# Kernel optimization log

Hardware: AMD Instinct MI355X
Metric: run time of the kernel (lower is better)

Reference implementation:

```python
import jax, jax.numpy as jnp
import numpy as np

H = 16        # num_heads
D = 64        # head_dim
HID = 1024    # hidden_size
WIN = 256     # window_size
GLOBAL = 0    # single global token index {0}


def _rope_tables(L):
    inv_freq = 1.0 / (10000.0 ** (jnp.arange(0, D, 2, dtype=jnp.float32) / D))
    pos = jnp.arange(L, dtype=jnp.float32)
    freqs = pos[:, None] * inv_freq[None, :]          # [L, D/2]
    emb = jnp.concatenate([freqs, freqs], axis=-1)     # [L, D]
    return jnp.cos(emb), jnp.sin(emb)


def _apply_rope(x, cos, sin):
    # x: [B, H, L, D]; cos/sin: [L, D]
    x1, x2 = x[..., : D // 2], x[..., D // 2 :]
    rot = jnp.concatenate([-x2, x1], axis=-1)
    return x * cos[None, None] + rot * sin[None, None]


def setup_inputs() -> dict:
    key = jax.random.key(0)
    ks = jax.random.split(key, 6)
    B, L = 2, 2048
    s = 0.02
    return {
        "hidden_states": jax.random.normal(ks[0], (B, L, HID), jnp.float32),
        "q_w": jax.random.normal(ks[1], (HID, HID), jnp.float32) * s,
        "q_b": jnp.zeros((HID,), jnp.float32),
        "k_w": jax.random.normal(ks[2], (HID, HID), jnp.float32) * s,
        "k_b": jnp.zeros((HID,), jnp.float32),
        "v_w": jax.random.normal(ks[3], (HID, HID), jnp.float32) * s,
        "v_b": jnp.zeros((HID,), jnp.float32),
        "o_w": jax.random.normal(ks[4], (HID, HID), jnp.float32) * s,
        "o_b": jnp.zeros((HID,), jnp.float32),
    }


def reference(hidden_states, q_w, q_b, k_w, k_b, v_w, v_b, o_w, o_b):
    B, L, _ = hidden_states.shape
    # torch Linear: y = x @ W^T + b
    q = hidden_states @ q_w.T + q_b
    k = hidden_states @ k_w.T + k_b
    v = hidden_states @ v_w.T + v_b
    # [B, L, H*D] -> [B, H, L, D]
    q = q.reshape(B, L, H, D).transpose(0, 2, 1, 3)
    k = k.reshape(B, L, H, D).transpose(0, 2, 1, 3)
    v = v.reshape(B, L, H, D).transpose(0, 2, 1, 3)

    cos, sin = _rope_tables(L)
    q = _apply_rope(q, cos, sin)
    k = _apply_rope(k, cos, sin)

    scale = jnp.float32(np.sqrt(D))
    scores = jnp.einsum("bhid,bhjd->bhij", q, k) / scale  # [B, H, L, L]

    # sparse mask: causal AND (within sliding window OR global token)
    i = jnp.arange(L)[:, None]
    j = jnp.arange(L)[None, :]
    keep = (j <= i) & (((i - j) < WIN) | (j == GLOBAL))    # [L, L] bool
    scores = jnp.where(keep[None, None], scores, jnp.float32(-jnp.inf))

    probs = jax.nn.softmax(scores, axis=-1)
    out = jnp.einsum("bhij,bhjd->bhid", probs, v)           # [B, H, L, D]
    out = out.transpose(0, 2, 1, 3).reshape(B, L, HID)
    return out @ o_w.T + o_b
```

## Files before the change

kernel.cpp:

```cpp
#include <hip/hip_runtime.h>
#include <hip/hip_bf16.h>
#include <cstdint>

#define LSEQ   2048
#define HID    1024
#define WIN    256
#define MROWS  4096

typedef unsigned short u16;
typedef unsigned int   u32;
typedef __attribute__((ext_vector_type(8))) short bf16x8;
typedef __attribute__((ext_vector_type(4))) float f32x4;
typedef __attribute__((address_space(1))) const unsigned int as1_uint;
typedef __attribute__((address_space(3))) unsigned int as3_uint;
typedef __attribute__((address_space(3))) char as3_char;

static __device__ __forceinline__ float bf2f(u16 u) {
  union { u32 u; float f; } c; c.u = ((u32)u) << 16; return c.f;
}
static __device__ __forceinline__ u16 f2bf(float f) {
  union { float f; u32 u; } c; c.f = f;
  u32 r = c.u + 0x7fffu + ((c.u >> 16) & 1u);
  return (u16)(r >> 16);
}

__global__ void cvt_all(const float* __restrict__ hidden,
                        const float* __restrict__ qw, const float* __restrict__ kw,
                        const float* __restrict__ vw, const float* __restrict__ ow,
                        u16* __restrict__ hbf, u16* __restrict__ wbf,
                        float* __restrict__ tab) {
  const int b = blockIdx.x;
  if (b >= 8192) {
    const int idx = (b - 8192) * 256 + threadIdx.x;
    const int l = idx >> 5, d = idx & 31;
    float invf = exp2f(-(float)d * (13.287712379549449f / 32.0f));
    float ang = (float)l * invf;
    tab[l * 64 + 2 * d]     = cosf(ang);
    tab[l * 64 + 2 * d + 1] = sinf(ang);
    return;
  }
  const int i = b * 256 + threadIdx.x;
  const float* src; u16* dst; int off;
  if (i < (1 << 20)) {
    src = hidden; dst = hbf; off = i;
  } else {
    const int j = i - (1 << 20);
    const int seg = j >> 18;
    off = j & ((1 << 18) - 1);
    src = (seg == 0) ? qw : (seg == 1) ? kw : (seg == 2) ? vw : ow;
    dst = wbf + ((size_t)seg << 20);
  }
  float4 v = ((const float4*)src)[off];
  u32 lo = (u32)f2bf(v.x) | ((u32)f2bf(v.y) << 16);
  u32 hi = (u32)f2bf(v.z) | ((u32)f2bf(v.w) << 16);
  ((uint2*)dst)[off] = make_uint2(lo, hi);
}

template<int NW>
__global__ __launch_bounds__(256, 2) void gemm_bt(
    const u16* __restrict__ A, const u16* __restrict__ W,
    const float* __restrict__ b0, const float* __restrict__ b1, const float* __restrict__ b2,
    u16* __restrict__ outb, float* __restrict__ outf, const float* __restrict__ tab,
    u16* __restrict__ vt)
{
  __shared__ u16 As[128 * 64];
  __shared__ u16 Bs[128 * 64];
  const int tid = threadIdx.x;
  const int lane = tid & 63, w = tid >> 6;
  const int wr = w >> 1, wc = w & 1;
  const int c = lane & 15, g = lane >> 4;

  const int GX = (NW == 3) ? 24 : 8;
  const int CH = (GX * 32) >> 3;
  int fid = blockIdx.y * GX + blockIdx.x;
  fid = (fid & 7) * CH + (fid >> 3);
  const int bx = fid % GX, by = fid / GX;

  const int srow = tid >> 3;
  const int scolb = ((tid & 7) * 16) ^ ((srow & 7) << 4);
  const char* gA = (const char*)(A + (size_t)(by * 128 + srow) * HID) + scolb;
  const char* gB = (const char*)(W + (size_t)(bx * 128 + srow) * HID) + scolb;

  f32x4 acc[4][4] = {};

  for (int kt = 0; kt < HID; kt += 64) {
    __syncthreads();
    #pragma unroll
    for (int r = 0; r < 4; ++r) {
      __builtin_amdgcn_global_load_lds((as1_uint*)(gA + kt * 2 + r * 32 * (HID * 2)),
                                       (as3_uint*)((as3_char*)As + r * 4096 + w * 1024), 16, 0, 0);
      __builtin_amdgcn_global_load_lds((as1_uint*)(gB + kt * 2 + r * 32 * (HID * 2)),
                                       (as3_uint*)((as3_char*)Bs + r * 4096 + w * 1024), 16, 0, 0);
    }
    __syncthreads();

    const int sw = (c & 7) << 4;
    #pragma unroll
    for (int ks = 0; ks < 2; ++ks) {
      const int colb = (g * 16 + ks * 64);
      bf16x8 af[4], bfr[4];
      #pragma unroll
      for (int mm = 0; mm < 4; ++mm) {
        const int row = wr * 64 + mm * 16 + c;
        af[mm] = *(const bf16x8*)((const char*)As + row * 128 + (colb ^ sw));
      }
      #pragma unroll
      for (int nn = 0; nn < 4; ++nn) {
        const int row = wc * 64 + nn * 16 + c;
        bfr[nn] = *(const bf16x8*)((const char*)Bs + row * 128 + (colb ^ sw));
      }
      #pragma unroll
      for (int mm = 0; mm < 4; ++mm)
        #pragma unroll
        for (int nn = 0; nn < 4; ++nn)
          acc[mm][nn] = __builtin_amdgcn_mfma_f32_16x16x32_bf16(af[mm], bfr[nn], acc[mm][nn], 0, 0, 0);
    }
  }

  const int which = (NW == 3) ? (bx >> 3) : 0;
  const float* bp = (NW == 3) ? (which == 0 ? b0 : (which == 1 ? b1 : b2)) : b0;
  const int cb = (NW == 3) ? ((bx & 7) * 128) : bx * 128;
  u16* ob_ = (NW == 3) ? (outb + (size_t)which * MROWS * HID) : (u16*)nullptr;
  const int rowg = by * 128 + wr * 64;

  #pragma unroll
  for (int nn = 0; nn < 4; ++nn) {
    const float bias = bp[cb + wc * 64 + nn * 16 + c];
    #pragma unroll
    for (int mm = 0; mm < 4; ++mm)
      #pragma unroll
      for (int r = 0; r < 4; ++r) acc[mm][nn][r] += bias;
  }

  if (NW == 3 && which < 2) {
    const float QS = (which == 0) ? (0.125f * 1.4426950408889634f) : 1.0f;
    #pragma unroll
    for (int mm = 0; mm < 4; ++mm) {
      #pragma unroll
      for (int r = 0; r < 4; ++r) {
        const int l = (rowg + mm * 16 + (g << 2) + r) & (LSEQ - 1);
        const float2* trow = (const float2*)(tab + l * 64);
        const float2 t0 = trow[c];
        const float2 t1 = trow[c + 16];
        const float x0 = acc[mm][0][r], y0 = acc[mm][2][r];
        const float x1 = acc[mm][1][r], y1 = acc[mm][3][r];
        acc[mm][0][r] = (x0 * t0.x - y0 * t0.y) * QS;
        acc[mm][2][r] = (y0 * t0.x + x0 * t0.y) * QS;
        acc[mm][1][r] = (x1 * t1.x - y1 * t1.y) * QS;
        acc[mm][3][r] = (y1 * t1.x + x1 * t1.y) * QS;
      }
    }
  }

  if (NW == 3 && which == 2) {
    #pragma unroll
    for (int nn = 0; nn < 4; ++nn) {
      const int cl = cb + wc * 64 + nn * 16 + c;
      const int hh = cl >> 6, hd = cl & 63;
      #pragma unroll
      for (int mm = 0; mm < 4; ++mm) {
        const int rb = rowg + mm * 16 + (g << 2);
        const int b_ = rb >> 11, l = rb & (LSEQ - 1);
        u16 t4[4];
        #pragma unroll
        for (int r = 0; r < 4; ++r) t4[r] = f2bf(acc[mm][nn][r]);
        *(uint2*)&vt[(size_t)((b_ * 16 + hh) * 64 + hd) * LSEQ + l] = *(uint2*)t4;
      }
    }
  } else {
    #pragma unroll
    for (int nn = 0; nn < 4; ++nn) {
      const int cl = cb + wc * 64 + nn * 16 + c;
      #pragma unroll
      for (int mm = 0; mm < 4; ++mm) {
        const int rb = rowg + mm * 16 + (g << 2);
        #pragma unroll
        for (int r = 0; r < 4; ++r) {
          if (NW == 3) ob_[(size_t)(rb + r) * HID + cl] = f2bf(acc[mm][nn][r]);
          else         outf[(size_t)(rb + r) * HID + cl] = acc[mm][nn][r];
        }
      }
    }
  }
}

__global__ __launch_bounds__(256) void attn_mfma(
    const u16* __restrict__ Q, const u16* __restrict__ K,
    const u16* __restrict__ Vt, u16* __restrict__ O)
{
  __shared__ u16 Ks[2 * 64 * 64];
  __shared__ u16 Vs[2 * 64 * 64];
  __shared__ u16 Ps[4 * 16 * 64];

  const int tid = threadIdx.x, lane = tid & 63, w = tid >> 6;
  const int g = lane >> 4, c = lane & 15;
  const int qb = (blockIdx.x & 31) * 64;
  const int bh = blockIdx.x >> 5;
  const int h = bh & 15;
  const size_t row0 = (size_t)(bh >> 4) * LSEQ;
  const int qw = qb + w * 16;

  const int srow = (w << 4) + (lane >> 3);
  const int scol = ((lane & 7) * 16) ^ ((lane >> 3) << 4);
  const char* gKb = (const char*)(K + (row0 + srow) * HID + h * 64) + scol;
  const char* gVb = (const char*)(Vt + (size_t)(bh * 64 + srow) * LSEQ) + scol;

  const u16* qptr = Q + (row0 + qw + c) * HID + h * 64 + g * 8;
  bf16x8 qa0 = *(const bf16x8*)qptr;
  bf16x8 qa1 = *(const bf16x8*)(qptr + 32);

  const int cbk = qb >> 6;
  int cf = (qb - (WIN - 1)) >> 6; if (cf < 0) cf = 0;

  float psum[4] = {0.f, 0.f, 0.f, 0.f};
  f32x4 o_[4];
  #pragma unroll
  for (int dt = 0; dt < 4; ++dt) o_[dt] = f32x4{0.f, 0.f, 0.f, 0.f};

  if (cf > 0) {
    const u16* k0p = K + row0 * HID + h * 64 + g * 8;
    bf16x8 k0a = *(const bf16x8*)k0p;
    bf16x8 k0b = *(const bf16x8*)(k0p + 32);
    float part = 0.f;
    #pragma unroll
    for (int j = 0; j < 8; ++j)
      part += bf2f((u16)qa0[j]) * bf2f((u16)k0a[j]) + bf2f((u16)qa1[j]) * bf2f((u16)k0b[j]);
    part += __shfl_xor(part, 16);
    part += __shfl_xor(part, 32);
    float p0 = exp2f(part);
    float prs[4];
    #pragma unroll
    for (int r = 0; r < 4; ++r) { prs[r] = __shfl(p0, g * 4 + r); psum[r] = prs[r]; }
    #pragma unroll
    for (int dt = 0; dt < 4; ++dt) {
      float v0 = bf2f(Vt[(size_t)(bh * 64 + dt * 16 + c) * LSEQ]);
      #pragma unroll
      for (int r = 0; r < 4; ++r) o_[dt][r] = prs[r] * v0;
    }
  }

  {
    const size_t kadv = (size_t)cf * 64 * 2048;
    const size_t vadv = (size_t)cf * 128;
    as3_char* lk = (as3_char*)Ks + w * 2048;
    as3_char* lv = (as3_char*)Vs + w * 2048;
    __builtin_amdgcn_global_load_lds((as1_uint*)(gKb + kadv),         (as3_uint*)lk,          16, 0, 0);
    __builtin_amdgcn_global_load_lds((as1_uint*)(gKb + kadv + 16384), (as3_uint*)(lk + 1024), 16, 0, 0);
    __builtin_amdgcn_global_load_lds((as1_uint*)(gVb + vadv),         (as3_uint*)lv,          16, 0, 0);
    __builtin_amdgcn_global_load_lds((as1_uint*)(gVb + vadv + 32768), (as3_uint*)(lv + 1024), 16, 0, 0);
  }

  int buf = 0;
  for (int ci = cf; ci <= cbk; ++ci) {
    const int c0 = ci * 64;
    __syncthreads();

    if (ci < cbk) {
      const size_t kadv = (size_t)(c0 + 64) * 2048;
      const size_t vadv = (size_t)(c0 + 64) * 2;
      as3_char* lk = (as3_char*)Ks + (buf ^ 1) * 8192 + w * 2048;
      as3_char* lv = (as3_char*)Vs + (buf ^ 1) * 8192 + w * 2048;
      __builtin_amdgcn_global_load_lds((as1_uint*)(gKb + kadv),         (as3_uint*)lk,          16, 0, 0);
      __builtin_amdgcn_global_load_lds((as1_uint*)(gKb + kadv + 16384), (as3_uint*)(lk + 1024), 16, 0, 0);
      __builtin_amdgcn_global_load_lds((as1_uint*)(gVb + vadv),         (as3_uint*)lv,          16, 0, 0);
      __builtin_amdgcn_global_load_lds((as1_uint*)(gVb + vadv + 32768), (as3_uint*)(lv + 1024), 16, 0, 0);
    }

    const char* ksbase = (const char*)Ks + buf * 8192;
    const char* vsbase = (const char*)Vs + buf * 8192;

    f32x4 st[4];
    #pragma unroll
    for (int t = 0; t < 4; ++t) {
      const int krow = t * 16 + c;
      const char* kbase = ksbase + krow * 128;
      const int sw = (krow & 7) << 4;
      bf16x8 kb0 = *(const bf16x8*)(kbase + ((g * 16) ^ sw));
      bf16x8 kb1 = *(const bf16x8*)(kbase + ((g * 16 + 64) ^ sw));
      st[t] = f32x4{0.f, 0.f, 0.f, 0.f};
      st[t] = __builtin_amdgcn_mfma_f32_16x16x32_bf16(qa0, kb0, st[t], 0, 0, 0);
      st[t] = __builtin_amdgcn_mfma_f32_16x16x32_bf16(qa1, kb1, st[t], 0, 0, 0);
    }

    float e[4][4];
    #pragma unroll
    for (int r = 0; r < 4; ++r) {
      const int qi = qw + g * 4 + r;
      #pragma unroll
      for (int t = 0; t < 4; ++t) {
        const int kj = c0 + t * 16 + c;
        const bool valid = (kj <= qi) && ((qi - kj < WIN) || (kj == 0));
        e[r][t] = valid ? exp2f(st[t][r]) : 0.f;
      }
      psum[r] += (e[r][0] + e[r][1]) + (e[r][2] + e[r][3]);
    }

    char* pwb = (char*)Ps + w * 2048;
    #pragma unroll
    for (int r = 0; r < 4; ++r) {
      const int q = g * 4 + r;
      char* prow = pwb + q * 128;
      const int sw = (q & 7) << 4;
      *(u16*)(prow + (((c + 0)  * 2) ^ sw)) = f2bf(e[r][0]);
      *(u16*)(prow + (((c + 16) * 2) ^ sw)) = f2bf(e[r][1]);
      *(u16*)(prow + (((c + 32) * 2) ^ sw)) = f2bf(e[r][2]);
      *(u16*)(prow + (((c + 48) * 2) ^ sw)) = f2bf(e[r][3]);
    }
    asm volatile("s_waitcnt lgkmcnt(0)" ::: "memory");
    __builtin_amdgcn_sched_barrier(0);

    bf16x8 pa[2];
    #pragma unroll
    for (int kh = 0; kh < 2; ++kh) {
      const int inner = (g * 16 + kh * 64) ^ ((c & 7) << 4);
      pa[kh] = *(const bf16x8*)(pwb + c * 128 + inner);
    }

    #pragma unroll
    for (int dt = 0; dt < 4; ++dt) {
      const int drow = dt * 16 + c;
      const char* vbase = vsbase + drow * 128;
      const int sw = (drow & 7) << 4;
      bf16x8 vb0 = *(const bf16x8*)(vbase + ((g * 16) ^ sw));
      bf16x8 vb1 = *(const bf16x8*)(vbase + ((g * 16 + 64) ^ sw));
      o_[dt] = __builtin_amdgcn_mfma_f32_16x16x32_bf16(pa[0], vb0, o_[dt], 0, 0, 0);
      o_[dt] = __builtin_amdgcn_mfma_f32_16x16x32_bf16(pa[1], vb1, o_[dt], 0, 0, 0);
    }
    buf ^= 1;
  }

  #pragma unroll
  for (int r = 0; r < 4; ++r) {
    #pragma unroll
    for (int off = 1; off < 16; off <<= 1) psum[r] += __shfl_xor(psum[r], off);
  }

  #pragma unroll
  for (int r = 0; r < 4; ++r) {
    const float inv = 1.f / psum[r];
    u16* orow = O + (row0 + qw + g * 4 + r) * HID + h * 64;
    #pragma unroll
    for (int dt = 0; dt < 4; ++dt)
      orow[dt * 16 + c] = f2bf(o_[dt][r] * inv);
  }
}

extern "C" void kernel_launch(void* const* d_in, const int* in_sizes, int n_in,
                              void* d_out, int out_size, void* d_ws, size_t ws_size,
                              hipStream_t stream) {
  const float* hidden = (const float*)d_in[0];
  const float* qw = (const float*)d_in[1];
  const float* qb = (const float*)d_in[2];
  const float* kw = (const float*)d_in[3];
  const float* kb = (const float*)d_in[4];
  const float* vw = (const float*)d_in[5];
  const float* vb = (const float*)d_in[6];
  const float* ow = (const float*)d_in[7];
  const float* ob = (const float*)d_in[8];
  float* out = (float*)d_out;

  u16* hbf = (u16*)d_ws;
  u16* wbf = hbf + (size_t)MROWS * HID;
  u16* qkv = wbf + (size_t)4 * HID * HID;
  float* tab = (float*)(qkv + (size_t)3 * MROWS * HID);
  u16* Vt = (u16*)(tab + (size_t)LSEQ * 64);

  cvt_all<<<8448, 256, 0, stream>>>(hidden, qw, kw, vw, ow, hbf, wbf, tab);

  gemm_bt<3><<<dim3(24, 32), 256, 0, stream>>>(hbf, wbf, qb, kb, vb, qkv, nullptr, tab, Vt);
  attn_mfma<<<1024, 256, 0, stream>>>(qkv, qkv + (size_t)MROWS * HID, Vt, qkv);
  gemm_bt<1><<<dim3(8, 32), 256, 0, stream>>>(qkv, wbf + (size_t)3 * HID * HID,
                                              ob, ob, ob, nullptr, out, nullptr, nullptr);
}
```

Measured before the change: 89.52 us.

## Replace QKV GEMM with 256x256-tile, 4-stage pipelined 8-wave kernel

The fused QKV projection now uses a dedicated kernel with 256x256 output tiles, 512 threads and 128KB of dynamic LDS. A 4-slot ring of K-chunks is prefetched two steps ahead with global_load_lds, and MFMA issue is interleaved with barriers and setprio. The goal is more data reuse per tile and overlap of global loads with matrix math. The trade-off is only 192 blocks on 256 CUs, the loss of the old LDS swizzle, which may cause bank conflicts, and heavy register and LDS pressure. The output GEMM is split into its own simplified kernel.

```diff
diff --git a/kernel.cpp b/kernel.cpp
--- a/kernel.cpp
+++ b/kernel.cpp
@@ -56,12 +56,152 @@
   ((uint2*)dst)[off] = make_uint2(lo, hi);
 }
 
-template<int NW>
-__global__ __launch_bounds__(256, 2) void gemm_bt(
+__global__ __launch_bounds__(512, 2) void gemm_qkv8(
     const u16* __restrict__ A, const u16* __restrict__ W,
     const float* __restrict__ b0, const float* __restrict__ b1, const float* __restrict__ b2,
-    u16* __restrict__ outb, float* __restrict__ outf, const float* __restrict__ tab,
-    u16* __restrict__ vt)
+    u16* __restrict__ outb, const float* __restrict__ tab, u16* __restrict__ vt)
+{
+  extern __shared__ u16 sm[];
+  const int tid = threadIdx.x;
+  const int lane = tid & 63, w = tid >> 6;
+  const int wr = w >> 2, wc = w & 3;
+  const int c = lane & 15, g = lane >> 4;
+
+  int fid = blockIdx.y * 12 + blockIdx.x;
+  fid = (fid & 7) * 24 + (fid >> 3);
+  const int bx = fid % 12, by = fid / 12;
+
+  const int srow = tid >> 2;
+  const int scolb = (tid & 3) * 16;
+  const char* gA = (const char*)A + ((size_t)(by * 256 + srow) * HID) * 2 + scolb;
+  const char* gB = (const char*)W + ((size_t)(bx * 256 + srow) * HID) * 2 + scolb;
+  as3_char* smb = (as3_char*)sm;
+
+#define STAGE_A(s, r) __builtin_amdgcn_global_load_lds( \
+    (as1_uint*)(gA + (size_t)(s) * 64 + (size_t)(r) * 128 * 2048), \
+    (as3_uint*)(smb + ((s) & 3) * 16384 + (r) * 8192 + w * 1024), 16, 0, 0)
+#define STAGE_B(s, r) __builtin_amdgcn_global_load_lds( \
+    (as1_uint*)(gB + (size_t)(s) * 64 + (size_t)(r) * 128 * 2048), \
+    (as3_uint*)(smb + 65536 + ((s) & 3) * 16384 + (r) * 8192 + w * 1024), 16, 0, 0)
+#define FENCE_BAR() do { \
+    asm volatile("" ::: "memory"); __builtin_amdgcn_sched_barrier(0); \
+    __builtin_amdgcn_s_barrier(); \
+    __builtin_amdgcn_sched_barrier(0); asm volatile("" ::: "memory"); } while (0)
+
+  f32x4 acc[8][4] = {};
+
+  STAGE_A(0, 0); STAGE_A(0, 1); STAGE_B(0, 0); STAGE_B(0, 1);
+  STAGE_A(1, 0); STAGE_A(1, 1); STAGE_B(1, 0); STAGE_B(1, 1);
+  asm volatile("s_waitcnt vmcnt(4)" ::: "memory");
+  __builtin_amdgcn_sched_barrier(0);
+  __builtin_amdgcn_s_barrier();
+  __builtin_amdgcn_sched_barrier(0);
+
+  for (int s = 0; s < 32; ++s) {
+    const int slotA = (s & 3) * 16384;
+    const int slotB = 65536 + (s & 3) * 16384;
+    #pragma unroll
+    for (int h2 = 0; h2 < 2; ++h2) {
+      bf16x8 af[4], bf[4];
+      #pragma unroll
+      for (int mm = 0; mm < 4; ++mm) {
+        const int row = wr * 128 + h2 * 64 + mm * 16 + c;
+        af[mm] = *(const bf16x8*)((const char*)sm + slotA + row * 64 + g * 16);
+      }
+      #pragma unroll
+      for (int nn = 0; nn < 4; ++nn) {
+        const int row = wc * 64 + nn * 16 + c;
+        bf[nn] = *(const bf16x8*)((const char*)sm + slotB + row * 64 + g * 16);
+      }
+      if (s + 2 < 32) {
+        if (h2 == 0) { STAGE_A(s + 2, 0); STAGE_A(s + 2, 1); }
+        else         { STAGE_B(s + 2, 0); STAGE_B(s + 2, 1); }
+      }
+      FENCE_BAR();
+      __builtin_amdgcn_s_setprio(1);
+      #pragma unroll
+      for (int mm = 0; mm < 4; ++mm)
+        #pragma unroll
+        for (int nn = 0; nn < 4; ++nn)
+          acc[h2 * 4 + mm][nn] =
+              __builtin_amdgcn_mfma_f32_16x16x32_bf16(af[mm], bf[nn], acc[h2 * 4 + mm][nn], 0, 0, 0);
+      __builtin_amdgcn_s_setprio(0);
+      if (h2 == 1) {
+        if (s + 2 < 32)      asm volatile("s_waitcnt vmcnt(4)" ::: "memory");
+        else if (s < 31)     asm volatile("s_waitcnt vmcnt(0)" ::: "memory");
+      }
+      FENCE_BAR();
+    }
+  }
+#undef STAGE_A
+#undef STAGE_B
+#undef FENCE_BAR
+
+  const int which = bx >> 2;
+  const float* bp = (which == 0) ? b0 : (which == 1 ? b1 : b2);
+  const int cmb = (bx & 3) * 256 + wc * 64;
+  const int hh = cmb >> 6;
+  u16* ob_ = outb + (size_t)which * MROWS * HID;
+  const int rowg = by * 256 + wr * 128;
+
+  #pragma unroll
+  for (int nn = 0; nn < 4; ++nn) {
+    const float bias = bp[cmb + nn * 16 + c];
+    #pragma unroll
+    for (int q = 0; q < 8; ++q)
+      #pragma unroll
+      for (int r = 0; r < 4; ++r) acc[q][nn][r] += bias;
+  }
+
+  if (which < 2) {
+    const float QS = (which == 0) ? (0.125f * 1.4426950408889634f) : 1.0f;
+    #pragma unroll
+    for (int q = 0; q < 8; ++q) {
+      #pragma unroll
+      for (int r = 0; r < 4; ++r) {
+        const int l = (rowg + (q >> 2) * 64 + (q & 3) * 16 + (g << 2) + r) & (LSEQ - 1);
+        const float2* trow = (const float2*)(tab + l * 64);
+        const float2 t0 = trow[c];
+        const float2 t1 = trow[c + 16];
+        const float x0 = acc[q][0][r], y0 = acc[q][2][r];
+        const float x1 = acc[q][1][r], y1 = acc[q][3][r];
+        acc[q][0][r] = (x0 * t0.x - y0 * t0.y) * QS;
+        acc[q][2][r] = (y0 * t0.x + x0 * t0.y) * QS;
+        acc[q][1][r] = (x1 * t1.x - y1 * t1.y) * QS;
+        acc[q][3][r] = (y1 * t1.x + x1 * t1.y) * QS;
+      }
+    }
+    #pragma unroll
+    for (int nn = 0; nn < 4; ++nn) {
+      const int cl = cmb + nn * 16 + c;
+      #pragma unroll
+      for (int q = 0; q < 8; ++q) {
+        const int rb = rowg + (q >> 2) * 64 + (q & 3) * 16 + (g << 2);
+        #pragma unroll
+        for (int r = 0; r < 4; ++r)
+          ob_[(size_t)(rb + r) * HID + cl] = f2bf(acc[q][nn][r]);
+      }
+    }
+  } else {
+    #pragma unroll
+    for (int nn = 0; nn < 4; ++nn) {
+      const int d = nn * 16 + c;
+      #pragma unroll
+      for (int q = 0; q < 8; ++q) {
+        const int rb = rowg + (q >> 2) * 64 + (q & 3) * 16 + (g << 2);
+        const int b_ = rb >> 11, l = rb & (LSEQ - 1);
+        u16 t4[4];
+        #pragma unroll
+        for (int r = 0; r < 4; ++r) t4[r] = f2bf(acc[q][nn][r]);
+        *(uint2*)&vt[(size_t)((b_ * 16 + hh) * 64 + d) * LSEQ + l] = *(uint2*)t4;
+      }
+    }
+  }
+}
+
+__global__ __launch_bounds__(256, 2) void gemm_o(
+    const u16* __restrict__ A, const u16* __restrict__ W,
+    const float* __restrict__ b0, float* __restrict__ outf)
 {
   __shared__ u16 As[128 * 64];
   __shared__ u16 Bs[128 * 64];
@@ -70,7 +210,7 @@
   const int wr = w >> 1, wc = w & 1;
   const int c = lane & 15, g = lane >> 4;
 
-  const int GX = (NW == 3) ? 24 : 8;
+  const int GX = 8;
   const int CH = (GX * 32) >> 3;
   int fid = blockIdx.y * GX + blockIdx.x;
   fid = (fid & 7) * CH + (fid >> 3);
@@ -117,69 +257,17 @@
     }
   }
 
-  const int which = (NW == 3) ? (bx >> 3) : 0;
-  const float* bp = (NW == 3) ? (which == 0 ? b0 : (which == 1 ? b1 : b2)) : b0;
-  const int cb = (NW == 3) ? ((bx & 7) * 128) : bx * 128;
-  u16* ob_ = (NW == 3) ? (outb + (size_t)which * MROWS * HID) : (u16*)nullptr;
   const int rowg = by * 128 + wr * 64;
-
   #pragma unroll
   for (int nn = 0; nn < 4; ++nn) {
-    const float bias = bp[cb + wc * 64 + nn * 16 + c];
-    #pragma unroll
-    for (int mm = 0; mm < 4; ++mm)
-      #pragma unroll
-      for (int r = 0; r < 4; ++r) acc[mm][nn][r] += bias;
-  }
-
-  if (NW == 3 && which < 2) {
-    const float QS = (which == 0) ? (0.125f * 1.4426950408889634f) : 1.0f;
+    const int cl = bx * 128 + wc * 64 + nn * 16 + c;
+    const float bias = b0[cl];
     #pragma unroll
     for (int mm = 0; mm < 4; ++mm) {
-      #pragma unroll
-      for (int r = 0; r < 4; ++r) {
-        const int l = (rowg + mm * 16 + (g << 2) + r) & (LSEQ - 1);
-        const float2* trow = (const float2*)(tab + l * 64);
-        const float2 t0 = trow[c];
-        const float2 t1 = trow[c + 16];
-        const float x0 = acc[mm][0][r], y0 = acc[mm][2][r];
-        const float x1 = acc[mm][1][r], y1 = acc[mm][3][r];
-        acc[mm][0][r] = (x0 * t0.x - y0 * t0.y) * QS;
-        acc[mm][2][r] = (y0 * t0.x + x0 * t0.y) * QS;
-        acc[mm][1][r] = (x1 * t1.x - y1 * t1.y) * QS;
-        acc[mm][3][r] = (y1 * t1.x + x1 * t1.y) * QS;
-      }
-    }
-  }
-
-  if (NW == 3 && which == 2) {
-    #pragma unroll
-    for (int nn = 0; nn < 4; ++nn) {
-      const int cl = cb + wc * 64 + nn * 16 + c;
-      const int hh = cl >> 6, hd = cl & 63;
-      #pragma unroll
-      for (int mm = 0; mm < 4; ++mm) {
-        const int rb = rowg + mm * 16 + (g << 2);
-        const int b_ = rb >> 11, l = rb & (LSEQ - 1);
-        u16 t4[4];
-        #pragma unroll
-        for (int r = 0; r < 4; ++r) t4[r] = f2bf(acc[mm][nn][r]);
-        *(uint2*)&vt[(size_t)((b_ * 16 + hh) * 64 + hd) * LSEQ + l] = *(uint2*)t4;
-      }
-    }
-  } else {
-    #pragma unroll
-    for (int nn = 0; nn < 4; ++nn) {
-      const int cl = cb + wc * 64 + nn * 16 + c;
-      #pragma unroll
-      for (int mm = 0; mm < 4; ++mm) {
-        const int rb = rowg + mm * 16 + (g << 2);
-        #pragma unroll
-        for (int r = 0; r < 4; ++r) {
-          if (NW == 3) ob_[(size_t)(rb + r) * HID + cl] = f2bf(acc[mm][nn][r]);
-          else         outf[(size_t)(rb + r) * HID + cl] = acc[mm][nn][r];
-        }
-      }
+      const int rb = rowg + mm * 16 + (g << 2);
+      #pragma unroll
+      for (int r = 0; r < 4; ++r)
+        outf[(size_t)(rb + r) * HID + cl] = acc[mm][nn][r] + bias;
     }
   }
 }
@@ -365,10 +453,12 @@
   float* tab = (float*)(qkv + (size_t)3 * MROWS * HID);
   u16* Vt = (u16*)(tab + (size_t)LSEQ * 64);
 
+  (void)hipFuncSetAttribute((const void*)gemm_qkv8,
+                            hipFuncAttributeMaxDynamicSharedMemorySize, 131072);
+
   cvt_all<<<8448, 256, 0, stream>>>(hidden, qw, kw, vw, ow, hbf, wbf, tab);
 
-  gemm_bt<3><<<dim3(24, 32), 256, 0, stream>>>(hbf, wbf, qb, kb, vb, qkv, nullptr, tab, Vt);
+  gemm_qkv8<<<dim3(12, 16), 512, 131072, stream>>>(hbf, wbf, qb, kb, vb, qkv, tab, Vt);
   attn_mfma<<<1024, 256, 0, stream>>>(qkv, qkv + (size_t)MROWS * HID, Vt, qkv);
-  gemm_bt<1><<<dim3(8, 32), 256, 0, stream>>>(qkv, wbf + (size_t)3 * HID * HID,
-                                              ob, ob, ob, nullptr, out, nullptr, nullptr);
-}
+  gemm_o<<<dim3(8, 32), 256, 0, stream>>>(qkv, wbf + (size_t)3 * HID * HID, ob, out);
+}
```

Result: slower. 98.29 us (+9.8%).
